# Kernel optimization log

Hardware: AMD Instinct MI355X
Metric: run time of the kernel (lower is better)

The kernel has to match this reference:

```python
import jax, jax.numpy as jnp
import numpy as np

N = 20000      # nodes
E = 80000      # edges (before self loops)
NG = 64        # graphs in batch
EMB = 780      # embedding_size (768 text + 12 time)
NEG_SLOPE = 0.2
BN_EPS = 1e-5


def setup_inputs() -> dict:
    key = jax.random.key(0)
    ks = jax.random.split(key, 20)
    def rn(k, shape, s=0.05):
        return jax.random.normal(k, shape, dtype=jnp.float32) * s
    z = lambda n: jnp.zeros((n,), dtype=jnp.float32)
    o = lambda n: jnp.ones((n,), dtype=jnp.float32)
    x = jax.random.normal(ks[0], (N, 772), dtype=jnp.float32)
    edge_index = jax.random.randint(ks[1], (2, E), 0, N)
    batch = jnp.sort(jax.random.randint(ks[2], (N,), 0, NG))
    return dict(
        x=x, edge_index=edge_index, batch=batch,
        time_W=rn(ks[3], (4, 12)), time_b=z(12),
        lin_W0=rn(ks[4], (EMB, 3 * EMB)), att_src0=rn(ks[5], (3, EMB)), att_dst0=rn(ks[6], (3, EMB)),
        bias0=z(3 * EMB), gamma0=o(3 * EMB), beta0=z(3 * EMB),
        lin_W1=rn(ks[7], (3 * EMB, 3 * EMB)), att_src1=rn(ks[8], (3, EMB)), att_dst1=rn(ks[9], (3, EMB)),
        bias1=z(3 * EMB), gamma1=o(3 * EMB), beta1=z(3 * EMB),
        lin_W2=rn(ks[10], (3 * EMB, EMB)), att_src2=rn(ks[11], (1, EMB)), att_dst2=rn(ks[12], (1, EMB)),
        bias2=z(EMB), gamma2=o(EMB), beta2=z(EMB),
        mlp_W1=rn(ks[13], (EMB, 128)), mlp_b1=z(128),
        mlp_W2=rn(ks[14], (128, 64)), mlp_b2=z(64),
    )


def _gat_layer(h, src, dst, W, a_src, a_dst, b, heads):
    # PyG GATConv (eval mode: dropout off), concat=True, self loops already in src/dst
    C = W.shape[1] // heads
    hp = (h @ W).reshape(N, heads, C)                       # [N,H,C]
    a_s = jnp.sum(hp * a_src[None], axis=-1)                # [N,H]
    a_d = jnp.sum(hp * a_dst[None], axis=-1)                # [N,H]
    e = jax.nn.leaky_relu(a_s[src] + a_d[dst], NEG_SLOPE)   # [E+N,H]
    m = jax.ops.segment_max(e, dst, num_segments=N)         # segment softmax over incoming edges
    m = jnp.where(jnp.isfinite(m), m, 0.0)
    p = jnp.exp(e - m[dst])
    denom = jax.ops.segment_sum(p, dst, num_segments=N)
    alpha = p / (denom[dst] + 1e-16)                        # [E+N,H]
    out = jax.ops.segment_sum(alpha[:, :, None] * hp[src], dst, num_segments=N)  # [N,H,C]
    return out.reshape(N, heads * C) + b


def _bn(h, gamma, beta):
    # BatchNorm in training-mode math (batch statistics, biased variance)
    mu = jnp.mean(h, axis=0)
    var = jnp.mean((h - mu) ** 2, axis=0)
    return (h - mu) * jax.lax.rsqrt(var + BN_EPS) * gamma + beta


def reference(x, edge_index, batch, time_W, time_b,
              lin_W0, att_src0, att_dst0, bias0, gamma0, beta0,
              lin_W1, att_src1, att_dst1, bias1, gamma1, beta1,
              lin_W2, att_src2, att_dst2, bias2, gamma2, beta2,
              mlp_W1, mlp_b1, mlp_W2, mlp_b2):
    te = x[:, 768:772] @ time_W + time_b
    h = jnp.concatenate([jax.lax.stop_gradient(x[:, :768]), te,
                         jax.lax.stop_gradient(x[:, 772:])], axis=-1)  # [N, 780]
    sl = jnp.arange(N)
    src = jnp.concatenate([edge_index[0], sl])   # add self loops
    dst = jnp.concatenate([edge_index[1], sl])
    layers = [
        (lin_W0, att_src0, att_dst0, bias0, gamma0, beta0, 3),
        (lin_W1, att_src1, att_dst1, bias1, gamma1, beta1, 3),
        (lin_W2, att_src2, att_dst2, bias2, gamma2, beta2, 1),
    ]
    for W, a_s, a_d, b, g, bt, heads in layers:
        h = jnp.tanh(_gat_layer(h, src, dst, W, a_s, a_d, b, heads))
        h = _bn(h, g, bt)
    cnt = jax.ops.segment_sum(jnp.ones((N,), dtype=h.dtype), batch, num_segments=NG)
    pooled = jax.ops.segment_sum(h, batch, num_segments=NG) / jnp.maximum(cnt, 1.0)[:, None]
    pooled = jax.nn.relu(pooled)
    out = jnp.tanh(pooled @ mlp_W1 + mlp_b1) @ mlp_W2 + mlp_b2
    return out  # [NG, 64]
```

## Files before the change

kernel.cpp:

```cpp
#include <hip/hip_runtime.h>
#include <math.h>

#define NN   20000
#define EE   80000
#define ELP  100000
#define NGR  64
#define EMB  780
#define W3   2340
#define EMBP 832
#define W3P  2368

static inline int cdiv_i(long long a, long long b){ return (int)((a + b - 1) / b); }

typedef _Float16 f16;
typedef _Float16 f16x4 __attribute__((ext_vector_type(4)));
typedef _Float16 f16x8 __attribute__((ext_vector_type(8)));
typedef float    f32x4 __attribute__((ext_vector_type(4)));

__device__ __forceinline__ void async_ld16(const f16* g, f16* l){
    __builtin_amdgcn_global_load_lds(
        (const __attribute__((address_space(1))) unsigned int*)g,
        (__attribute__((address_space(3))) unsigned int*)l,
        16, 0, 0);
}

__global__ void k_zero_f32(float* p, int n){
    int i = blockIdx.x*256 + threadIdx.x; if (i < n) p[i] = 0.f;
}
__global__ void k_zero_i32(int* p, int n){
    int i = blockIdx.x*256 + threadIdx.x; if (i < n) p[i] = 0;
}
__global__ void k_copy_i32(const int* __restrict__ s, int* __restrict__ d, int n){
    int i = blockIdx.x*256 + threadIdx.x; if (i < n) d[i] = s[i];
}

__global__ void k_transpose(const float* __restrict__ W, f16* __restrict__ Wt,
                            const float* __restrict__ sc, int K, int N, int KP){
    __shared__ float T[32][33];
    int n0 = blockIdx.x*32, k0 = blockIdx.y*32;
    int tx = threadIdx.x, ty = threadIdx.y;
#pragma unroll
    for (int r = 0; r < 4; r++){
        int k = k0 + ty + r*8;
        float v = 0.f;
        if (k < K && n0 + tx < N){
            v = W[(size_t)k*N + n0 + tx];
            if (sc) v *= sc[k];
        }
        T[ty + r*8][tx] = v;
    }
    __syncthreads();
#pragma unroll
    for (int r = 0; r < 4; r++){
        int n = n0 + ty + r*8;
        int k = k0 + tx;
        if (n < N && k < KP) Wt[(size_t)n*KP + k] = (f16)T[tx][ty + r*8];
    }
}

#define DVEC_KSPLIT 32
__global__ void k_dvec(const float* __restrict__ W, const float* __restrict__ sh,
                       float* __restrict__ dvec, int K, int N){
    int n = blockIdx.x*256 + threadIdx.x;
    if (n >= N) return;
    int slice = blockIdx.y;
    int k0 = (int)(((long long)K * slice) / DVEC_KSPLIT);
    int k1 = (int)(((long long)K * (slice+1)) / DVEC_KSPLIT);
    float s = 0.f;
    for (int k = k0; k < k1; k++) s += sh[k] * W[(size_t)k*N + n];
    atomicAdd(&dvec[n], s);
}

__global__ void k_build_h(const float* __restrict__ x, const float* __restrict__ tW,
                          const float* __restrict__ tb, f16* __restrict__ h){
    int idx = blockIdx.x*256 + threadIdx.x;
    if (idx >= NN*EMBP) return;
    int n = idx / EMBP, c = idx - n*EMBP;
    const float* xr = x + (size_t)n*772;
    float v;
    if (c < 768) v = xr[c];
    else if (c < EMB){
        int j = c - 768;
        v = tb[j] + xr[768]*tW[j] + xr[769]*tW[12+j] + xr[770]*tW[24+j] + xr[771]*tW[36+j];
    } else v = 0.f;
    h[idx] = (f16)v;
}

__global__ void k_deg(const int* __restrict__ ei, int* __restrict__ deg){
    int k = blockIdx.x*256 + threadIdx.x; if (k >= ELP) return;
    int d = (k < EE) ? ei[EE + k] : (k - EE);
    atomicAdd(&deg[d], 1);
}

__global__ __launch_bounds__(1024) void k_scan(const int* __restrict__ deg, int* __restrict__ rp){
    __shared__ int part[1024];
    int tid = threadIdx.x;
    int i0 = tid*20;
    int n = (i0 < NN) ? min(20, NN - i0) : 0;
    int s = 0;
    for (int k = 0; k < n; k++) s += deg[i0+k];
    part[tid] = s; __syncthreads();
    for (int off = 1; off < 1024; off <<= 1){
        int t = (tid >= off) ? part[tid-off] : 0;
        __syncthreads();
        part[tid] += t;
        __syncthreads();
    }
    int run = part[tid] - s;
    for (int k = 0; k < n; k++){ rp[i0+k] = run; run += deg[i0+k]; }
    if (tid == 1023) rp[NN] = part[1023];
}

__global__ void k_fill(const int* __restrict__ ei, int* __restrict__ cursor, int* __restrict__ csrc){
    int k = blockIdx.x*256 + threadIdx.x; if (k >= ELP) return;
    int s, d;
    if (k < EE){ s = ei[k]; d = ei[EE + k]; } else { s = k - EE; d = s; }
    int pos = atomicAdd(&cursor[d], 1);
    csrc[pos] = s;
}

__global__ void k_grp(const int* __restrict__ batch, int* __restrict__ grp){
    int g = blockIdx.x*256 + threadIdx.x; if (g > NGR) return;
    int lo = 0, hi = NN;
    while (lo < hi){ int mid = (lo+hi)>>1; if (batch[mid] < g) lo = mid+1; else hi = mid; }
    grp[g] = lo;
}

__global__ __launch_bounds__(256) void k_gemm_mfma(const f16* __restrict__ A,
                                                   const f16* __restrict__ Bt,
                                                   const float* __restrict__ dvec,
                                                   f16* __restrict__ C,
                                                   int M, int N, int KP, int SN,
                                                   int Mtiles, int NT){
    int bid = blockIdx.x;
    int xcd = bid & 7;
    int j   = bid >> 3;
    int sl  = j / NT;
    int nt  = j - sl*NT;
    int mt  = sl*8 + xcd;
    if (mt >= Mtiles) return;
    int m0 = mt*128, n0 = nt*128;

    __shared__ f16 As[128*64];
    __shared__ f16 Bs[128*64];
    int tid = threadIdx.x;
    int w = tid >> 6, lane = tid & 63;

    int lrow = lane >> 2;
    int lko  = (lane & 3) * 8;

    int i2a = w*2, i2b = w*2 + 1;
    const f16* gA0 = A  + (size_t)min(m0 + i2a*16 + lrow, M-1)*KP + lko;
    const f16* gA1 = A  + (size_t)min(m0 + i2b*16 + lrow, M-1)*KP + lko;
    const f16* gB0 = Bt + (size_t)min(n0 + i2a*16 + lrow, N-1)*KP + lko;
    const f16* gB1 = Bt + (size_t)min(n0 + i2b*16 + lrow, N-1)*KP + lko;
    f16* lA0 = &As[i2a*512]; f16* lA1 = &As[i2b*512];
    f16* lB0 = &Bs[i2a*512]; f16* lB1 = &Bs[i2b*512];

    f32x4 acc[4][4];
#pragma unroll
    for (int i = 0; i < 4; i++)
#pragma unroll
        for (int j2 = 0; j2 < 4; j2++) acc[i][j2] = (f32x4)0.f;

    int wm = (w & 1) * 64, wn = (w >> 1) * 64;
    int lq = lane >> 4, lm = lane & 15;

    for (int kk = 0; kk < KP; kk += 64){
        __syncthreads();
        async_ld16(gA0 + kk, lA0);
        async_ld16(gA1 + kk, lA1);
        async_ld16(gB0 + kk, lB0);
        async_ld16(gB1 + kk, lB1);
        async_ld16(gA0 + kk + 32, lA0 + 4096);
        async_ld16(gA1 + kk + 32, lA1 + 4096);
        async_ld16(gB0 + kk + 32, lB0 + 4096);
        async_ld16(gB1 + kk + 32, lB1 + 4096);
        __syncthreads();

#pragma unroll
        for (int half = 0; half < 2; half++){
            const f16* Ap = As + half*4096;
            const f16* Bp = Bs + half*4096;
            f16x8 aF[4], bF[4];
#pragma unroll
            for (int mi = 0; mi < 4; mi++)
                aF[mi] = *(const f16x8*)&Ap[(wm + mi*16 + lm)*32 + lq*8];
#pragma unroll
            for (int ni = 0; ni < 4; ni++)
                bF[ni] = *(const f16x8*)&Bp[(wn + ni*16 + lm)*32 + lq*8];
#pragma unroll
            for (int mi = 0; mi < 4; mi++)
#pragma unroll
                for (int ni = 0; ni < 4; ni++)
                    acc[mi][ni] = __builtin_amdgcn_mfma_f32_16x16x32_f16(aF[mi], bF[ni], acc[mi][ni], 0, 0, 0);
        }
    }

#pragma unroll
    for (int mi = 0; mi < 4; mi++){
#pragma unroll
        for (int ni = 0; ni < 4; ni++){
            int col = n0 + wn + ni*16 + lm;
            if (col < SN){
                float dv = (col < N) ? dvec[col] : 0.f;
                int rbase = m0 + wm + mi*16 + lq*4;
#pragma unroll
                for (int r = 0; r < 4; r++){
                    int row = rbase + r;
                    if (row < M){
                        float v = (col < N) ? (acc[mi][ni][r] + dv) : 0.f;
                        C[(size_t)row*SN + col] = (f16)v;
                    }
                }
            }
        }
    }
}

__global__ void k_att(const f16* __restrict__ hp, const float* __restrict__ asrc,
                      const float* __restrict__ adst, float* __restrict__ a_s,
                      float* __restrict__ a_d, int H, int SP){
    int n = blockIdx.x;
    int wv = threadIdx.x >> 6, lane = threadIdx.x & 63;
    const f16* row = hp + (size_t)n*SP + wv*EMB;
    const float* pa = asrc + wv*EMB;
    const float* pd = adst + wv*EMB;
    float s = 0.f, d = 0.f;
    for (int c = lane*4; c < EMB; c += 256){
        f16x4 v = *(const f16x4*)(row + c);
#pragma unroll
        for (int jj = 0; jj < 4; jj++){
            float f = (float)v[jj];
            s += f*pa[c+jj]; d += f*pd[c+jj];
        }
    }
#pragma unroll
    for (int off = 32; off; off >>= 1){ s += __shfl_xor(s, off); d += __shfl_xor(d, off); }
    if (lane == 0){ a_s[n*H + wv] = s; a_d[n*H + wv] = d; }
}

__global__ __launch_bounds__(256) void k_agg(const f16* __restrict__ hp, const int* __restrict__ rp,
                                             const int* __restrict__ csrc, const float* __restrict__ a_s,
                                             const float* __restrict__ a_d, const float* __restrict__ bias,
                                             f16* __restrict__ y, int H, int SP, int W){
    int n = blockIdx.x, tid = threadIdx.x;
    int beg = rp[n], deg = rp[n+1] - beg;

    __shared__ float sm[3], sden[3];
    __shared__ float sal[64*3];
    __shared__ int   ssrc[64];

    if (tid < 64){
        float adn[3];
#pragma unroll
        for (int h = 0; h < 3; h++) adn[h] = (h < H) ? a_d[n*H + h] : 0.f;
        float mx[3] = {-1e30f, -1e30f, -1e30f};
        for (int e = tid; e < deg; e += 64){
            int s = csrc[beg + e];
#pragma unroll
            for (int h = 0; h < 3; h++) if (h < H){
                float v = a_s[s*H + h] + adn[h];
                v = v > 0.f ? v : 0.2f*v;
                mx[h] = fmaxf(mx[h], v);
            }
        }
#pragma unroll
        for (int off = 32; off; off >>= 1){
#pragma unroll
            for (int h = 0; h < 3; h++) mx[h] = fmaxf(mx[h], __shfl_xor(mx[h], off));
        }
        float dn[3] = {0.f, 0.f, 0.f};
        for (int e = tid; e < deg; e += 64){
            int s = csrc[beg + e];
#pragma unroll
            for (int h = 0; h < 3; h++) if (h < H){
                float v = a_s[s*H + h] + adn[h];
                v = v > 0.f ? v : 0.2f*v;
                dn[h] += expf(v - mx[h]);
            }
        }
#pragma unroll
        for (int off = 32; off; off >>= 1){
#pragma unroll
            for (int h = 0; h < 3; h++) dn[h] += __shfl_xor(dn[h], off);
        }
        if (tid == 0){
#pragma unroll
            for (int h = 0; h < 3; h++){ sm[h] = mx[h]; sden[h] = dn[h]; }
        }
    }
    __syncthreads();

    float4 acc4[3];
    int c4[3], hh4[3];
#pragma unroll
    for (int i = 0; i < 3; i++){
        acc4[i] = make_float4(0.f,0.f,0.f,0.f);
        c4[i] = tid*4 + i*1024;
        hh4[i] = (c4[i] < W) ? (c4[i] / EMB) : 0;
    }

    for (int base = 0; base < deg; base += 64){
        int cnt = min(64, deg - base);
        if (tid < cnt) ssrc[tid] = csrc[beg + base + tid];
        if (tid < cnt*H){
            int e = tid / H, h = tid - e*H;
            int s = csrc[beg + base + e];
            float v = a_s[s*H + h] + a_d[n*H + h];
            v = v > 0.f ? v : 0.2f*v;
            sal[e*3 + h] = expf(v - sm[h]) / (sden[h] + 1e-16f);
        }
        __syncthreads();
        int e = 0;
        for (; e + 2 <= cnt; e += 2){
            const f16* r0 = hp + (size_t)ssrc[e]*SP;
            const f16* r1 = hp + (size_t)ssrc[e+1]*SP;
            f16x4 va[3], vb[3];
#pragma unroll
            for (int i = 0; i < 3; i++)
                if (c4[i] < W){
                    va[i] = *(const f16x4*)(r0 + c4[i]);
                    vb[i] = *(const f16x4*)(r1 + c4[i]);
                }
#pragma unroll
            for (int i = 0; i < 3; i++)
                if (c4[i] < W){
                    float a0 = sal[e*3 + hh4[i]], a1 = sal[(e+1)*3 + hh4[i]];
                    acc4[i].x += a0*(float)va[i][0] + a1*(float)vb[i][0];
                    acc4[i].y += a0*(float)va[i][1] + a1*(float)vb[i][1];
                    acc4[i].z += a0*(float)va[i][2] + a1*(float)vb[i][2];
                    acc4[i].w += a0*(float)va[i][3] + a1*(float)vb[i][3];
                }
        }
        if (e < cnt){
            const f16* r0 = hp + (size_t)ssrc[e]*SP;
#pragma unroll
            for (int i = 0; i < 3; i++)
                if (c4[i] < W){
                    f16x4 v = *(const f16x4*)(r0 + c4[i]);
                    float al = sal[e*3 + hh4[i]];
                    acc4[i].x += al*(float)v[0];
                    acc4[i].y += al*(float)v[1];
                    acc4[i].z += al*(float)v[2];
                    acc4[i].w += al*(float)v[3];
                }
        }
        __syncthreads();
    }

#pragma unroll
    for (int i = 0; i < 3; i++){
        int c = c4[i];
        if (c < SP){
            f16x4 o;
            if (c < W){
                o[0] = (f16)tanhf(acc4[i].x + bias[c]);
                o[1] = (f16)tanhf(acc4[i].y + bias[c+1]);
                o[2] = (f16)tanhf(acc4[i].z + bias[c+2]);
                o[3] = (f16)tanhf(acc4[i].w + bias[c+3]);
            } else { o[0]=(f16)0.f; o[1]=(f16)0.f; o[2]=(f16)0.f; o[3]=(f16)0.f; }
            *(f16x4*)(y + (size_t)n*SP + c) = o;
        }
    }
}

__global__ void k_bnstat(const f16* __restrict__ y, float* __restrict__ ps,
                         float* __restrict__ pq, int W, int SP){
    int c0 = (blockIdx.x*256 + threadIdx.x)*4;
    if (c0 >= W) return;
    int slice = blockIdx.y;
    float s[4] = {0,0,0,0}, q[4] = {0,0,0,0};
    for (int r = slice; r < NN; r += 64){
        f16x4 u = *(const f16x4*)(y + (size_t)r*SP + c0);
#pragma unroll
        for (int j = 0; j < 4; j++){ float v = (float)u[j]; s[j] += v; q[j] += v*v; }
    }
#pragma unroll
    for (int j = 0; j < 4; j++){
        ps[(size_t)slice*W3 + c0+j] = s[j];
        pq[(size_t)slice*W3 + c0+j] = q[j];
    }
}

__global__ void k_bnfin(const float* __restrict__ ps, const float* __restrict__ pq,
                        const float* __restrict__ gamma, const float* __restrict__ beta,
                        float* __restrict__ sc, float* __restrict__ sh, int W){
    int c = blockIdx.x*256 + threadIdx.x; if (c >= W) return;
    float m = 0.f, q = 0.f;
    for (int s = 0; s < 64; s++){ m += ps[(size_t)s*W3 + c]; q += pq[(size_t)s*W3 + c]; }
    m *= (1.f/NN);
    float v = q * (1.f/NN) - m*m;
    float is = 1.f / sqrtf(v + 1e-5f);
    float g = gamma[c];
    sc[c] = is * g;
    sh[c] = beta[c] - m * is * g;
}

__global__ void k_pool(const f16* __restrict__ h, const int* __restrict__ grp,
                       float* __restrict__ pooled){
    int g = blockIdx.x;
    int c = blockIdx.y*256 + threadIdx.x;
    if (c >= EMB) return;
    int r0 = grp[g], r1 = grp[g+1];
    float s = 0.f;
    for (int r = r0; r < r1; r++) s += (float)h[(size_t)r*EMBP + c];
    pooled[g*EMB + c] = s;
}

__global__ __launch_bounds__(256) void k_mlp(const float* __restrict__ pooled, const int* __restrict__ grp,
                                             const float* __restrict__ sc, const float* __restrict__ sh,
                                             const float* __restrict__ W1, const float* __restrict__ b1,
                                             const float* __restrict__ W2, const float* __restrict__ b2,
                                             float* __restrict__ out){
    __shared__ float p[EMB];
    __shared__ float hid[128];
    int g = blockIdx.x, tid = threadIdx.x;
    int cnt = grp[g+1] - grp[g];
    float ic = 1.f / fmaxf((float)cnt, 1.f);
    for (int c = tid; c < EMB; c += 256){
        float v = pooled[g*EMB + c] * ic * sc[c] + sh[c];
        p[c] = v > 0.f ? v : 0.f;
    }
    __syncthreads();
    if (tid < 128){
        float s = b1[tid];
        for (int k = 0; k < EMB; k++) s += p[k] * W1[k*128 + tid];
        hid[tid] = tanhf(s);
    }
    __syncthreads();
    if (tid < 64){
        float s = b2[tid];
        for (int k = 0; k < 128; k++) s += hid[k] * W2[k*64 + tid];
        out[g*64 + tid] = s;
    }
}

extern "C" void kernel_launch(void* const* d_in, const int* in_sizes, int n_in,
                              void* d_out, int out_size, void* d_ws, size_t ws_size,
                              hipStream_t stream) {
    (void)in_sizes; (void)n_in; (void)out_size;
    const float* x    = (const float*)d_in[0];
    const int*   ei   = (const int*)  d_in[1];
    const int*   batch= (const int*)  d_in[2];
    const float* tW   = (const float*)d_in[3];
    const float* tb   = (const float*)d_in[4];
    const float* W0   = (const float*)d_in[5];
    const float* as0  = (const float*)d_in[6];
    const float* ad0  = (const float*)d_in[7];
    const float* b0   = (const float*)d_in[8];
    const float* g0   = (const float*)d_in[9];
    const float* be0  = (const float*)d_in[10];
    const float* W1   = (const float*)d_in[11];
    const float* as1  = (const float*)d_in[12];
    const float* ad1  = (const float*)d_in[13];
    const float* b1   = (const float*)d_in[14];
    const float* g1   = (const float*)d_in[15];
    const float* be1  = (const float*)d_in[16];
    const float* W2   = (const float*)d_in[17];
    const float* as2  = (const float*)d_in[18];
    const float* ad2  = (const float*)d_in[19];
    const float* b2   = (const float*)d_in[20];
    const float* g2   = (const float*)d_in[21];
    const float* be2  = (const float*)d_in[22];
    const float* mW1  = (const float*)d_in[23];
    const float* mb1  = (const float*)d_in[24];
    const float* mW2  = (const float*)d_in[25];
    const float* mb2  = (const float*)d_in[26];
    float* outp = (float*)d_out;

    size_t off = 0;
    auto carve = [&](size_t bytes) -> void* {
        void* p = (char*)d_ws + off;
        off = (off + bytes + 255) & ~(size_t)255;
        return p;
    };
    f16* big1 = (f16*)carve((size_t)NN*W3P*2);
    f16* big2 = (f16*)carve((size_t)NN*W3P*2);
    f16* Wt   = (f16*)carve((size_t)W3*W3P*2);
    float* a_s   = (float*)carve((size_t)NN*3*4);
    float* a_d   = (float*)carve((size_t)NN*3*4);
    float* psum  = (float*)carve((size_t)64*W3*4);
    float* psq   = (float*)carve((size_t)64*W3*4);
    float* sc    = (float*)carve((size_t)W3*4);
    float* sh    = (float*)carve((size_t)W3*4);
    float* dvec  = (float*)carve((size_t)W3*4);
    float* pooled= (float*)carve((size_t)NGR*EMB*4);
    int*   grp   = (int*)carve((size_t)(NGR+1)*4);
    int*   deg   = (int*)carve((size_t)NN*4);
    int*   rp    = (int*)carve((size_t)(NN+1)*4);
    int*   csrc  = (int*)carve((size_t)ELP*4);

    if (ws_size < off) return;

    k_zero_i32<<<cdiv_i(NN,256),256,0,stream>>>(deg, NN);
    k_deg<<<cdiv_i(ELP,256),256,0,stream>>>(ei, deg);
    k_scan<<<1,1024,0,stream>>>(deg, rp);
    k_copy_i32<<<cdiv_i(NN,256),256,0,stream>>>(rp, deg, NN);
    k_fill<<<cdiv_i(ELP,256),256,0,stream>>>(ei, deg, csrc);
    k_grp<<<1,256,0,stream>>>(batch, grp);

    k_build_h<<<cdiv_i((long long)NN*EMBP,256),256,0,stream>>>(x, tW, tb, big1);

    struct Layer { const float* W; const float* as; const float* ad; const float* b;
                   const float* g; const float* be; int H; int K; int KP; };
    Layer layers[3] = {
        {W0, as0, ad0, b0, g0, be0, 3, EMB, EMBP},
        {W1, as1, ad1, b1, g1, be1, 3, W3,  W3P },
        {W2, as2, ad2, b2, g2, be2, 1, W3,  W3P },
    };

    for (int L = 0; L < 3; L++){
        Layer& ly = layers[L];
        int Wout  = ly.H * EMB;
        int SPout = (Wout == W3) ? W3P : EMBP;
        const float* scale = (L == 0) ? nullptr : sc;

        dim3 tg(cdiv_i(Wout,32), cdiv_i(ly.KP,32));
        k_transpose<<<tg, dim3(32,8), 0, stream>>>(ly.W, Wt, scale, ly.K, Wout, ly.KP);
        k_zero_f32<<<cdiv_i(W3,256),256,0,stream>>>(dvec, W3);
        if (L > 0){
            dim3 dg(cdiv_i(Wout,256), DVEC_KSPLIT);
            k_dvec<<<dg,256,0,stream>>>(ly.W, sh, dvec, ly.K, Wout);
        }

        int Mtiles = cdiv_i(NN,128), NT = cdiv_i(Wout,128);
        int nb = ((Mtiles+7)/8)*8*NT;
        k_gemm_mfma<<<nb, 256, 0, stream>>>(big1, Wt, dvec, big2, NN, Wout, ly.KP, SPout, Mtiles, NT);

        k_att<<<NN, ly.H*64, 0, stream>>>(big2, ly.as, ly.ad, a_s, a_d, ly.H, SPout);

        k_agg<<<NN,256,0,stream>>>(big2, rp, csrc, a_s, a_d, ly.b, big1, ly.H, SPout, Wout);

        dim3 gs(cdiv_i(Wout/4,256), 64);
        k_bnstat<<<gs,256,0,stream>>>(big1, psum, psq, Wout, SPout);
        k_bnfin<<<cdiv_i(Wout,256),256,0,stream>>>(psum, psq, ly.g, ly.be, sc, sh, Wout);
    }

    dim3 pg(NGR, cdiv_i(EMB,256));
    k_pool<<<pg,256,0,stream>>>(big1, grp, pooled);
    k_mlp<<<NGR,256,0,stream>>>(pooled, grp, sc, sh, mW1, mb1, mW2, mb2, outp);
}
```

Before: 1.667 ms.

## Rewrite GAT aggregation with per-wave softmax, shuffles and 8-wide loads

The aggregation kernel is now templated on head count. Every wave computes the segment max and denominator redundantly in its own registers, then broadcasts edge sources and attention weights through wave shuffles instead of shared memory. This removes the block-wide barriers and shared-memory staging, and each thread loads 8 halves per row instead of 4. The pooling kernel is also vectorized to read 4 halves per thread. The cost is redundant softmax work across the four waves and extra per-element select logic where an 8-wide group crosses a head boundary.

```diff
diff --git a/kernel.cpp b/kernel.cpp
--- a/kernel.cpp
+++ b/kernel.cpp
@@ -240,127 +240,130 @@
     if (lane == 0){ a_s[n*H + wv] = s; a_d[n*H + wv] = d; }
 }
 
-__global__ __launch_bounds__(256) void k_agg(const f16* __restrict__ hp, const int* __restrict__ rp,
-                                             const int* __restrict__ csrc, const float* __restrict__ a_s,
-                                             const float* __restrict__ a_d, const float* __restrict__ bias,
-                                             f16* __restrict__ y, int H, int SP, int W){
-    int n = blockIdx.x, tid = threadIdx.x;
+template<int H>
+__global__ __launch_bounds__(256) void k_agg2(const f16* __restrict__ hp, const int* __restrict__ rp,
+                                              const int* __restrict__ csrc, const float* __restrict__ a_s,
+                                              const float* __restrict__ a_d, const float* __restrict__ bias,
+                                              f16* __restrict__ y, int SP, int W){
+    int n = blockIdx.x, tid = threadIdx.x, lane = tid & 63;
     int beg = rp[n], deg = rp[n+1] - beg;
 
-    __shared__ float sm[3], sden[3];
-    __shared__ float sal[64*3];
-    __shared__ int   ssrc[64];
-
-    if (tid < 64){
-        float adn[3];
-#pragma unroll
-        for (int h = 0; h < 3; h++) adn[h] = (h < H) ? a_d[n*H + h] : 0.f;
-        float mx[3] = {-1e30f, -1e30f, -1e30f};
-        for (int e = tid; e < deg; e += 64){
+    float adv[H];
+#pragma unroll
+    for (int h = 0; h < H; h++) adv[h] = a_d[n*H + h];
+
+    float mx[H];
+#pragma unroll
+    for (int h = 0; h < H; h++) mx[h] = -1e30f;
+    for (int base = 0; base < deg; base += 64){
+        int e = base + lane;
+        if (e < deg){
             int s = csrc[beg + e];
 #pragma unroll
-            for (int h = 0; h < 3; h++) if (h < H){
-                float v = a_s[s*H + h] + adn[h];
-                v = v > 0.f ? v : 0.2f*v;
-                mx[h] = fmaxf(mx[h], v);
+            for (int h = 0; h < H; h++){
+                float t = a_s[s*H + h] + adv[h];
+                t = t > 0.f ? t : 0.2f*t;
+                mx[h] = fmaxf(mx[h], t);
             }
         }
-#pragma unroll
-        for (int off = 32; off; off >>= 1){
-#pragma unroll
-            for (int h = 0; h < 3; h++) mx[h] = fmaxf(mx[h], __shfl_xor(mx[h], off));
-        }
-        float dn[3] = {0.f, 0.f, 0.f};
-        for (int e = tid; e < deg; e += 64){
+    }
+#pragma unroll
+    for (int off = 32; off; off >>= 1)
+#pragma unroll
+        for (int h = 0; h < H; h++) mx[h] = fmaxf(mx[h], __shfl_xor(mx[h], off));
+
+    float dn[H];
+#pragma unroll
+    for (int h = 0; h < H; h++) dn[h] = 0.f;
+    for (int base = 0; base < deg; base += 64){
+        int e = base + lane;
+        if (e < deg){
             int s = csrc[beg + e];
 #pragma unroll
-            for (int h = 0; h < 3; h++) if (h < H){
-                float v = a_s[s*H + h] + adn[h];
-                v = v > 0.f ? v : 0.2f*v;
-                dn[h] += expf(v - mx[h]);
+            for (int h = 0; h < H; h++){
+                float t = a_s[s*H + h] + adv[h];
+                t = t > 0.f ? t : 0.2f*t;
+                dn[h] += expf(t - mx[h]);
             }
         }
-#pragma unroll
-        for (int off = 32; off; off >>= 1){
-#pragma unroll
-            for (int h = 0; h < 3; h++) dn[h] += __shfl_xor(dn[h], off);
-        }
-        if (tid == 0){
-#pragma unroll
-            for (int h = 0; h < 3; h++){ sm[h] = mx[h]; sden[h] = dn[h]; }
-        }
-    }
-    __syncthreads();
-
-    float4 acc4[3];
-    int c4[3], hh4[3];
-#pragma unroll
-    for (int i = 0; i < 3; i++){
-        acc4[i] = make_float4(0.f,0.f,0.f,0.f);
-        c4[i] = tid*4 + i*1024;
-        hh4[i] = (c4[i] < W) ? (c4[i] / EMB) : 0;
+    }
+#pragma unroll
+    for (int off = 32; off; off >>= 1)
+#pragma unroll
+        for (int h = 0; h < H; h++) dn[h] += __shfl_xor(dn[h], off);
+    float inv[H];
+#pragma unroll
+    for (int h = 0; h < H; h++) inv[h] = 1.f / (dn[h] + 1e-16f);
+
+    float acc[2][8];
+#pragma unroll
+    for (int g = 0; g < 2; g++)
+#pragma unroll
+        for (int j = 0; j < 8; j++) acc[g][j] = 0.f;
+    int  cg[2];  cg[0] = tid*8; cg[1] = 2048 + tid*8;
+    bool act[2]; act[0] = cg[0] < W; act[1] = cg[1] < W;
+    int hlo[2], hhi[2], nsp[2];
+#pragma unroll
+    for (int g = 0; g < 2; g++){
+        int c = cg[g];
+        int hl = min(c / EMB, H-1);
+        int hh = min((c+7) / EMB, H-1);
+        hlo[g] = hl; hhi[g] = hh;
+        nsp[g] = (hh > hl) ? (EMB*(hl+1) - c) : 8;
     }
 
     for (int base = 0; base < deg; base += 64){
         int cnt = min(64, deg - base);
-        if (tid < cnt) ssrc[tid] = csrc[beg + base + tid];
-        if (tid < cnt*H){
-            int e = tid / H, h = tid - e*H;
-            int s = csrc[beg + base + e];
-            float v = a_s[s*H + h] + a_d[n*H + h];
-            v = v > 0.f ? v : 0.2f*v;
-            sal[e*3 + h] = expf(v - sm[h]) / (sden[h] + 1e-16f);
-        }
-        __syncthreads();
-        int e = 0;
-        for (; e + 2 <= cnt; e += 2){
-            const f16* r0 = hp + (size_t)ssrc[e]*SP;
-            const f16* r1 = hp + (size_t)ssrc[e+1]*SP;
-            f16x4 va[3], vb[3];
-#pragma unroll
-            for (int i = 0; i < 3; i++)
-                if (c4[i] < W){
-                    va[i] = *(const f16x4*)(r0 + c4[i]);
-                    vb[i] = *(const f16x4*)(r1 + c4[i]);
+        int sl = 0; float al[H];
+        {
+            int e = base + lane;
+            if (e < deg){
+                sl = csrc[beg + e];
+#pragma unroll
+                for (int h = 0; h < H; h++){
+                    float t = a_s[sl*H + h] + adv[h];
+                    t = t > 0.f ? t : 0.2f*t;
+                    al[h] = expf(t - mx[h]) * inv[h];
                 }
-#pragma unroll
-            for (int i = 0; i < 3; i++)
-                if (c4[i] < W){
-                    float a0 = sal[e*3 + hh4[i]], a1 = sal[(e+1)*3 + hh4[i]];
-                    acc4[i].x += a0*(float)va[i][0] + a1*(float)vb[i][0];
-                    acc4[i].y += a0*(float)va[i][1] + a1*(float)vb[i][1];
-                    acc4[i].z += a0*(float)va[i][2] + a1*(float)vb[i][2];
-                    acc4[i].w += a0*(float)va[i][3] + a1*(float)vb[i][3];
+            } else {
+#pragma unroll
+                for (int h = 0; h < H; h++) al[h] = 0.f;
+            }
+        }
+#pragma unroll 2
+        for (int e = 0; e < cnt; e++){
+            int s = __shfl(sl, e);
+            float a0 = __shfl(al[0], e);
+            float a1 = (H==3) ? __shfl(al[1], e) : a0;
+            float a2 = (H==3) ? __shfl(al[2], e) : a0;
+            const f16* row = hp + (size_t)s*SP;
+#pragma unroll
+            for (int g = 0; g < 2; g++){
+                if (act[g]){
+                    f16x8 v = *(const f16x8*)(row + cg[g]);
+                    float lo = (hlo[g]==0) ? a0 : (hlo[g]==1 ? a1 : a2);
+                    float hi = (hhi[g]==0) ? a0 : (hhi[g]==1 ? a1 : a2);
+#pragma unroll
+                    for (int j = 0; j < 8; j++){
+                        float alj = (j < nsp[g]) ? lo : hi;
+                        acc[g][j] += alj * (float)v[j];
+                    }
                 }
-        }
-        if (e < cnt){
-            const f16* r0 = hp + (size_t)ssrc[e]*SP;
-#pragma unroll
-            for (int i = 0; i < 3; i++)
-                if (c4[i] < W){
-                    f16x4 v = *(const f16x4*)(r0 + c4[i]);
-                    float al = sal[e*3 + hh4[i]];
-                    acc4[i].x += al*(float)v[0];
-                    acc4[i].y += al*(float)v[1];
-                    acc4[i].z += al*(float)v[2];
-                    acc4[i].w += al*(float)v[3];
-                }
-        }
-        __syncthreads();
-    }
-
-#pragma unroll
-    for (int i = 0; i < 3; i++){
-        int c = c4[i];
+            }
+        }
+    }
+
+#pragma unroll
+    for (int g = 0; g < 2; g++){
+        int c = cg[g];
         if (c < SP){
-            f16x4 o;
-            if (c < W){
-                o[0] = (f16)tanhf(acc4[i].x + bias[c]);
-                o[1] = (f16)tanhf(acc4[i].y + bias[c+1]);
-                o[2] = (f16)tanhf(acc4[i].z + bias[c+2]);
-                o[3] = (f16)tanhf(acc4[i].w + bias[c+3]);
-            } else { o[0]=(f16)0.f; o[1]=(f16)0.f; o[2]=(f16)0.f; o[3]=(f16)0.f; }
-            *(f16x4*)(y + (size_t)n*SP + c) = o;
+            f16x8 o;
+#pragma unroll
+            for (int j = 0; j < 8; j++){
+                float vv = (c + j < W) ? tanhf(acc[g][j] + bias[c+j]) : 0.f;
+                o[j] = (f16)vv;
+            }
+            *(f16x8*)(y + (size_t)n*SP + c) = o;
         }
     }
 }
@@ -400,12 +403,16 @@
 __global__ void k_pool(const f16* __restrict__ h, const int* __restrict__ grp,
                        float* __restrict__ pooled){
     int g = blockIdx.x;
-    int c = blockIdx.y*256 + threadIdx.x;
+    int c = threadIdx.x*4;
     if (c >= EMB) return;
     int r0 = grp[g], r1 = grp[g+1];
-    float s = 0.f;
-    for (int r = r0; r < r1; r++) s += (float)h[(size_t)r*EMBP + c];
-    pooled[g*EMB + c] = s;
+    float s0=0.f, s1=0.f, s2=0.f, s3=0.f;
+    for (int r = r0; r < r1; r++){
+        f16x4 u = *(const f16x4*)(h + (size_t)r*EMBP + c);
+        s0 += (float)u[0]; s1 += (float)u[1]; s2 += (float)u[2]; s3 += (float)u[3];
+    }
+    pooled[g*EMB + c] = s0; pooled[g*EMB + c+1] = s1;
+    pooled[g*EMB + c+2] = s2; pooled[g*EMB + c+3] = s3;
 }
 
 __global__ __launch_bounds__(256) void k_mlp(const float* __restrict__ pooled, const int* __restrict__ grp,
@@ -530,14 +537,16 @@
 
         k_att<<<NN, ly.H*64, 0, stream>>>(big2, ly.as, ly.ad, a_s, a_d, ly.H, SPout);
 
-        k_agg<<<NN,256,0,stream>>>(big2, rp, csrc, a_s, a_d, ly.b, big1, ly.H, SPout, Wout);
+        if (ly.H == 3)
+            k_agg2<3><<<NN,256,0,stream>>>(big2, rp, csrc, a_s, a_d, ly.b, big1, SPout, Wout);
+        else
+            k_agg2<1><<<NN,256,0,stream>>>(big2, rp, csrc, a_s, a_d, ly.b, big1, SPout, Wout);
 
         dim3 gs(cdiv_i(Wout/4,256), 64);
         k_bnstat<<<gs,256,0,stream>>>(big1, psum, psq, Wout, SPout);
         k_bnfin<<<cdiv_i(Wout,256),256,0,stream>>>(psum, psq, ly.g, ly.be, sc, sh, Wout);
     }
 
-    dim3 pg(NGR, cdiv_i(EMB,256));
-    k_pool<<<pg,256,0,stream>>>(big1, grp, pooled);
+    k_pool<<<NGR,256,0,stream>>>(big1, grp, pooled);
     k_mlp<<<NGR,256,0,stream>>>(pooled, grp, sc, sh, mW1, mb1, mW2, mb2, outp);
 }
```

Result: no change. 1.678 ms (+0.7%).
